# Optimization experiments

Measured on AMD Instinct MI355X. Metric: run time of the kernel, lower is better.

Reference implementation:

```python
import jax, jax.numpy as jnp
import numpy as np

BN_EPS = 1e-5


def knn_idx(x, k):
    # x: (B, N, C) -> (B, N, k) indices of k nearest neighbors (incl. self),
    # DGCNN style: topk of negative squared distance.
    inner = jnp.einsum('bnc,bmc->bnm', x, x)
    sq = jnp.sum(x * x, axis=-1)
    neg_dist = 2.0 * inner - sq[:, :, None] - sq[:, None, :]
    _, idx = jax.lax.top_k(neg_dist, k)
    return idx


def edge_conv(x, W, b, gamma, beta, k):
    # x: (B, N, C); W: (O, 2C). One DGCNN EdgeConv block:
    # knn gather -> concat(nbr - x, x) -> conv1x1 -> BN(batch stats) -> GELU -> max over k.
    idx = knn_idx(x, k)                                   # (B, N, k)
    nbr = jax.vmap(lambda f, i: f[i])(x, idx)             # (B, N, k, C)
    ctr = jnp.broadcast_to(x[:, :, None, :], nbr.shape)
    feat = jnp.concatenate([nbr - ctr, ctr], axis=-1)     # (B, N, k, 2C)
    y = jnp.einsum('bnkc,oc->bnko', feat, W) + b          # conv 1x1
    mean = jnp.mean(y, axis=(0, 1, 2))
    var = jnp.var(y, axis=(0, 1, 2))
    y = (y - mean) * jax.lax.rsqrt(var + BN_EPS) * gamma + beta
    y = jax.nn.gelu(y, approximate=False)                 # torch nn.GELU default (erf)
    return jnp.max(y, axis=2)                             # (B, N, O)


def setup_inputs() -> dict:
    key = jax.random.key(0)
    ks = jax.random.split(key, 8)
    bs, ch, n_patches, n_samples = 4, 6, 32, 256
    dims_in = [12, 32, 64, 128, 256]
    dims_out = [16, 32, 64, 128, 256]
    inp = {'x': jax.random.normal(ks[0], (bs, ch, n_patches, n_samples), dtype=jnp.float32)}
    for i, (ci, co) in enumerate(zip(dims_in, dims_out), start=1):
        wk = jax.random.fold_in(ks[1], i)
        scale = 1.0 / np.sqrt(ci)
        inp[f'W{i}'] = (jax.random.normal(wk, (co, ci), dtype=jnp.float32) * scale)
        inp[f'b{i}'] = jnp.zeros((co,), dtype=jnp.float32)
        inp[f'g{i}'] = jnp.ones((co,), dtype=jnp.float32)
        inp[f'bt{i}'] = jnp.zeros((co,), dtype=jnp.float32)
    inp['k'] = 16
    return inp


def reference(x, W1, b1, g1, bt1, W2, b2, g2, bt2, W3, b3, g3, bt3,
              W4, b4, g4, bt4, W5, b5, g5, bt5, k):
    bs, ch, n_patches, n_samples = x.shape
    # (bs, ch, P, S) -> (bs*P, S, ch)  [channels-last point clouds]
    h = x.transpose(0, 2, 3, 1).reshape(bs * n_patches, n_samples, ch)
    h = edge_conv(h, W1, b1, g1, bt1, k)
    h = edge_conv(h, W2, b2, g2, bt2, k)
    h = edge_conv(h, W3, b3, g3, bt3, k)
    h = edge_conv(h, W4, b4, g4, bt4, k)
    h = edge_conv(h, W5, b5, g5, bt5, k)      # (bs*P, S, dim)
    dim = h.shape[-1]
    h = h.reshape(bs, n_patches, n_samples, dim)
    return h.transpose(0, 3, 1, 2)            # (bs, dim, n_patches, n_samples)
```

## Files before the change

### kernel.cpp

```cpp
#include <hip/hip_runtime.h>
#include <cmath>

#define NPTS 256
#define TOTPTS 32768
#define KNB 16

static const size_t OFF_HA   = 0;
static const size_t OFF_HB   = 4194304;
static const size_t OFF_UZ   = 6291456;
static const size_t OFF_YMAX = 23068672;
static const size_t OFF_YMIN = 31457280;
static const size_t OFF_IDX  = 39845888;
static const size_t OFF_VT   = 40370176;
static const size_t OFF_SUMS = 40458240;

__device__ __forceinline__ float gelu_erf(float v) {
  return 0.5f * v * (1.0f + erff(v * 0.70710678118654752f));
}

__global__ __launch_bounds__(256) void prep_kernel(
    const float* __restrict__ x, float* __restrict__ h0,
    const float* __restrict__ W1, const float* __restrict__ W2, const float* __restrict__ W3,
    const float* __restrict__ W4, const float* __restrict__ W5,
    float* __restrict__ Vt, double* __restrict__ sums) {
  const int stride = gridDim.x * blockDim.x;
  const int tid0 = blockIdx.x * blockDim.x + threadIdx.x;
  for (int id = tid0; id < 196608; id += stride) {
    int ch = id % 6;
    int r  = id / 6;
    int s  = r & 255;
    int p  = (r >> 8) & 31;
    int bs = r >> 13;
    h0[id] = x[(((size_t)(bs * 6 + ch) * 32 + p) << 8) + s];
  }
  for (int id = tid0; id < 87232; id += stride) {
    const float* W; int K, N2, base;
    if (id < 192)        { W = W1; K = 6;   N2 = 32;  base = 0; }
    else if (id < 1216)  { W = W2; K = 16;  N2 = 64;  base = 192; }
    else if (id < 5312)  { W = W3; K = 32;  N2 = 128; base = 1216; }
    else if (id < 21696) { W = W4; K = 64;  N2 = 256; base = 5312; }
    else                 { W = W5; K = 128; N2 = 512; base = 21696; }
    int e = id - base;
    int c = e / N2;
    int j = e - c * N2;
    int O = N2 >> 1;
    Vt[id] = (j < O) ? W[j * 2 * K + c] : W[(j - O) * 2 * K + K + c];
  }
  for (int id = tid0; id < 992; id += stride) sums[id] = 0.0;
}

template<int C>
__global__ __launch_bounds__(256) void sq_kernel(const float* __restrict__ h,
                                                 double* __restrict__ sqd) {
  const int n = blockIdx.x * 256 + threadIdx.x;
  const float* p = h + (size_t)n * C;
  double q0 = 0.0, q1 = 0.0;
  #pragma unroll
  for (int c = 0; c + 1 < C; c += 2) {
    q0 = fma((double)p[c],   (double)p[c],   q0);
    q1 = fma((double)p[c+1], (double)p[c+1], q1);
  }
  #pragma unroll
  for (int c = C & ~1; c < C; ++c) q0 = fma((double)p[c], (double)p[c], q0);
  sqd[n] = q0 + q1;
}

template<int K>
__global__ __launch_bounds__(256) void knn_fused_kernel(const float* __restrict__ h,
                                                        const double* __restrict__ sqd,
                                                        int* __restrict__ idxout) {
  constexpr int KC  = (K < 16) ? K : 16;
  constexpr int AST = 18;
  constexpr int BST = 260;
  __shared__ __align__(16) float As[KC * AST];
  __shared__ __align__(16) float Bs[KC * BST];
  const int xcd   = blockIdx.x & 7;
  const int q     = blockIdx.x >> 3;
  const int cloud = xcd + 8 * (q >> 4);
  const int strip = q & 15;
  const int i0    = strip * 16;
  const float* hb = h + (size_t)cloud * NPTS * K;
  const int tid = threadIdx.x;
  const int c   = tid & 31;
  const int g   = tid >> 5;

  double acc[2][8];
  #pragma unroll
  for (int r = 0; r < 2; ++r)
    #pragma unroll
    for (int j = 0; j < 8; ++j) acc[r][j] = 0.0;

  for (int k0 = 0; k0 < K; k0 += KC) {
    if (K >= 16) {
      {
        int am = tid >> 4, ac = tid & 15;
        As[ac * AST + am] = hb[(size_t)(i0 + am) * K + k0 + ac];
      }
      #pragma unroll
      for (int qq = 0; qq < 4; ++qq) {
        int idx = tid + 256 * qq;
        int j  = idx >> 2;
        int kq = idx & 3;
        float4 v = *(const float4*)(hb + (size_t)j * K + k0 + 4 * kq);
        Bs[(4 * kq + 0) * BST + j] = v.x;
        Bs[(4 * kq + 1) * BST + j] = v.y;
        Bs[(4 * kq + 2) * BST + j] = v.z;
        Bs[(4 * kq + 3) * BST + j] = v.w;
      }
    } else {
      for (int e = tid; e < 16 * KC; e += 256) {
        int am = e / KC, ac = e - am * KC;
        As[ac * AST + am] = hb[(size_t)(i0 + am) * K + ac];
      }
      for (int e = tid; e < 256 * KC; e += 256) {
        int bm = e / KC, bc = e - bm * KC;
        Bs[bc * BST + bm] = hb[(size_t)bm * K + bc];
      }
    }
    __syncthreads();
    #pragma unroll
    for (int kk = 0; kk < KC; ++kk) {
      float2 af  = *(const float2*)(As + kk * AST + 2 * g);
      float4 bf0 = *(const float4*)(Bs + kk * BST + 4 * c);
      float4 bf1 = *(const float4*)(Bs + kk * BST + 128 + 4 * c);
      double a0 = (double)af.x, a1 = (double)af.y;
      double b0 = (double)bf0.x, b1 = (double)bf0.y, b2 = (double)bf0.z, b3 = (double)bf0.w;
      double b4 = (double)bf1.x, b5 = (double)bf1.y, b6 = (double)bf1.z, b7 = (double)bf1.w;
      acc[0][0] = fma(a0, b0, acc[0][0]);
      acc[0][1] = fma(a0, b1, acc[0][1]);
      acc[0][2] = fma(a0, b2, acc[0][2]);
      acc[0][3] = fma(a0, b3, acc[0][3]);
      acc[0][4] = fma(a0, b4, acc[0][4]);
      acc[0][5] = fma(a0, b5, acc[0][5]);
      acc[0][6] = fma(a0, b6, acc[0][6]);
      acc[0][7] = fma(a0, b7, acc[0][7]);
      acc[1][0] = fma(a1, b0, acc[1][0]);
      acc[1][1] = fma(a1, b1, acc[1][1]);
      acc[1][2] = fma(a1, b2, acc[1][2]);
      acc[1][3] = fma(a1, b3, acc[1][3]);
      acc[1][4] = fma(a1, b4, acc[1][4]);
      acc[1][5] = fma(a1, b5, acc[1][5]);
      acc[1][6] = fma(a1, b6, acc[1][6]);
      acc[1][7] = fma(a1, b7, acc[1][7]);
    }
    __syncthreads();
  }

  const double sqi0 = sqd[cloud * NPTS + i0 + 2 * g];
  const double sqi1 = sqd[cloud * NPTS + i0 + 2 * g + 1];
  double sqj[8];
  #pragma unroll
  for (int e = 0; e < 4; ++e) {
    sqj[e]     = sqd[cloud * NPTS + 4 * c + e];
    sqj[4 + e] = sqd[cloud * NPTS + 128 + 4 * c + e];
  }
  const unsigned cb0 = 4u * (unsigned)c;
  const unsigned cb1 = 128u + 4u * (unsigned)c;

  #define MK(P, COLV) ((((unsigned long long)__double_as_longlong(P)) & ~0xFFull) | (COLV))
  unsigned long long a0 = MK(2.0 * acc[0][0] - sqi0 - sqj[0], cb0 + 0u);
  unsigned long long a1 = MK(2.0 * acc[0][1] - sqi0 - sqj[1], cb0 + 1u);
  unsigned long long a2 = MK(2.0 * acc[0][2] - sqi0 - sqj[2], cb0 + 2u);
  unsigned long long a3 = MK(2.0 * acc[0][3] - sqi0 - sqj[3], cb0 + 3u);
  unsigned long long a4 = MK(2.0 * acc[0][4] - sqi0 - sqj[4], cb1 + 0u);
  unsigned long long a5 = MK(2.0 * acc[0][5] - sqi0 - sqj[5], cb1 + 1u);
  unsigned long long a6 = MK(2.0 * acc[0][6] - sqi0 - sqj[6], cb1 + 2u);
  unsigned long long a7 = MK(2.0 * acc[0][7] - sqi0 - sqj[7], cb1 + 3u);
  unsigned long long b0 = MK(2.0 * acc[1][0] - sqi1 - sqj[0], cb0 + 0u);
  unsigned long long b1 = MK(2.0 * acc[1][1] - sqi1 - sqj[1], cb0 + 1u);
  unsigned long long b2 = MK(2.0 * acc[1][2] - sqi1 - sqj[2], cb0 + 2u);
  unsigned long long b3 = MK(2.0 * acc[1][3] - sqi1 - sqj[3], cb0 + 3u);
  unsigned long long b4 = MK(2.0 * acc[1][4] - sqi1 - sqj[4], cb1 + 0u);
  unsigned long long b5 = MK(2.0 * acc[1][5] - sqi1 - sqj[5], cb1 + 1u);
  unsigned long long b6 = MK(2.0 * acc[1][6] - sqi1 - sqj[6], cb1 + 2u);
  unsigned long long b7 = MK(2.0 * acc[1][7] - sqi1 - sqj[7], cb1 + 3u);
  #undef MK

  #define CE(X, Y) { unsigned long long lo_ = (X < Y) ? X : Y; \
                     unsigned long long hi_ = (X < Y) ? Y : X; X = lo_; Y = hi_; }
  #define SORT8(v0,v1,v2,v3,v4,v5,v6,v7) \
    CE(v0,v1) CE(v2,v3) CE(v4,v5) CE(v6,v7) \
    CE(v0,v2) CE(v1,v3) CE(v4,v6) CE(v5,v7) \
    CE(v1,v2) CE(v5,v6) \
    CE(v0,v4) CE(v1,v5) CE(v2,v6) CE(v3,v7) \
    CE(v2,v4) CE(v3,v5) \
    CE(v1,v2) CE(v3,v4) CE(v5,v6)
  SORT8(a0,a1,a2,a3,a4,a5,a6,a7)
  SORT8(b0,b1,b2,b3,b4,b5,b6,b7)
  #undef SORT8
  #undef CE

  const unsigned long long FULL = 0xFFFFFFFFFFFFFFFFull;
  const int sub = c;
  int keep1 = 0, keep2 = 0;
  for (int round = 0; round < KNB; ++round) {
    unsigned long long m1 = a0, m2 = b0, o;
    o = __shfl_xor(m1, 16); m1 = (o < m1) ? o : m1;
    o = __shfl_xor(m2, 16); m2 = (o < m2) ? o : m2;
    o = __shfl_xor(m1, 8);  m1 = (o < m1) ? o : m1;
    o = __shfl_xor(m2, 8);  m2 = (o < m2) ? o : m2;
    o = __shfl_xor(m1, 4);  m1 = (o < m1) ? o : m1;
    o = __shfl_xor(m2, 4);  m2 = (o < m2) ? o : m2;
    o = __shfl_xor(m1, 2);  m1 = (o < m1) ? o : m1;
    o = __shfl_xor(m2, 2);  m2 = (o < m2) ? o : m2;
    o = __shfl_xor(m1, 1);  m1 = (o < m1) ? o : m1;
    o = __shfl_xor(m2, 1);  m2 = (o < m2) ? o : m2;
    const int col1 = (int)(m1 & 0xFFull);
    const int col2 = (int)(m2 & 0xFFull);
    if (((col1 >> 2) & 31) == sub) {
      a0 = a1; a1 = a2; a2 = a3; a3 = a4; a4 = a5; a5 = a6; a6 = a7; a7 = FULL;
    }
    if (((col2 >> 2) & 31) == sub) {
      b0 = b1; b1 = b2; b2 = b3; b3 = b4; b4 = b5; b5 = b6; b6 = b7; b7 = FULL;
    }
    if (sub == round) { keep1 = col1; keep2 = col2; }
  }
  if (sub < KNB) {
    const int rowA = cloud * NPTS + i0 + 2 * g;
    idxout[(size_t)rowA * KNB + sub]       = cloud * NPTS + keep1;
    idxout[(size_t)(rowA + 1) * KNB + sub] = cloud * NPTS + keep2;
  }
}

template<int K, int N2>
__global__ __launch_bounds__(256) void gemm_uz_kernel(const float* __restrict__ h,
                                                      const float* __restrict__ Vt,
                                                      float* __restrict__ UZ) {
  constexpr int KC = 32;
  constexpr int NBLK = (N2 + 63) / 64;
  __shared__ __align__(16) float As[KC * 68];
  __shared__ __align__(16) float Bs[KC * 68];
  const int m0 = (int)(blockIdx.x / NBLK) * 64;
  const int n0 = (int)(blockIdx.x % NBLK) * 64;
  const int tid = threadIdx.x;
  const int mm = (tid & 15) * 4;
  const int jj = (tid >> 4) * 4;
  float acc[4][4] = {{0.f}};
  for (int k0 = 0; k0 < K; k0 += KC) {
    #pragma unroll
    for (int e = tid; e < 64 * KC; e += 256) {
      int am = e / KC, ac = e - am * KC;
      float v = 0.f;
      if (k0 + ac < K) v = h[(size_t)(m0 + am) * K + k0 + ac];
      As[ac * 68 + am] = v;
    }
    #pragma unroll
    for (int e = tid; e < KC * 64; e += 256) {
      int bj = e & 63, bc = e >> 6;
      float v = 0.f;
      if (k0 + bc < K && n0 + bj < N2) v = Vt[(size_t)(k0 + bc) * N2 + n0 + bj];
      Bs[bc * 68 + bj] = v;
    }
    __syncthreads();
    #pragma unroll
    for (int c = 0; c < KC; ++c) {
      float4 av = *(const float4*)(As + c * 68 + mm);
      float4 bv = *(const float4*)(Bs + c * 68 + jj);
      acc[0][0] = fmaf(av.x, bv.x, acc[0][0]);
      acc[0][1] = fmaf(av.x, bv.y, acc[0][1]);
      acc[0][2] = fmaf(av.x, bv.z, acc[0][2]);
      acc[0][3] = fmaf(av.x, bv.w, acc[0][3]);
      acc[1][0] = fmaf(av.y, bv.x, acc[1][0]);
      acc[1][1] = fmaf(av.y, bv.y, acc[1][1]);
      acc[1][2] = fmaf(av.y, bv.z, acc[1][2]);
      acc[1][3] = fmaf(av.y, bv.w, acc[1][3]);
      acc[2][0] = fmaf(av.z, bv.x, acc[2][0]);
      acc[2][1] = fmaf(av.z, bv.y, acc[2][1]);
      acc[2][2] = fmaf(av.z, bv.z, acc[2][2]);
      acc[2][3] = fmaf(av.z, bv.w, acc[2][3]);
      acc[3][0] = fmaf(av.w, bv.x, acc[3][0]);
      acc[3][1] = fmaf(av.w, bv.y, acc[3][1]);
      acc[3][2] = fmaf(av.w, bv.z, acc[3][2]);
      acc[3][3] = fmaf(av.w, bv.w, acc[3][3]);
    }
    __syncthreads();
  }
  if (n0 + jj < N2) {
    #pragma unroll
    for (int i = 0; i < 4; ++i) {
      float4 v = make_float4(acc[i][0], acc[i][1], acc[i][2], acc[i][3]);
      *(float4*)(UZ + (size_t)(m0 + mm + i) * N2 + n0 + jj) = v;
    }
  }
}

template<int K, int N2>
__global__ __launch_bounds__(256) void gemm_big_kernel(const float* __restrict__ h,
                                                       const float* __restrict__ Vt,
                                                       float* __restrict__ UZ) {
  constexpr int KC = 32;
  constexpr int PAD = 132;
  constexpr int NBLK = N2 / 128;
  __shared__ __align__(16) float As[KC * PAD];
  __shared__ __align__(16) float Bs[KC * PAD];
  const int m0 = (int)(blockIdx.x / NBLK) * 128;
  const int n0 = (int)(blockIdx.x % NBLK) * 128;
  const int tid = threadIdx.x;
  const int ra = (tid & 15) * 4;
  const int ca = (tid >> 4) * 4;
  float acc[8][8];
  #pragma unroll
  for (int i = 0; i < 8; ++i)
    #pragma unroll
    for (int j = 0; j < 8; ++j) acc[i][j] = 0.f;

  for (int k0 = 0; k0 < K; k0 += KC) {
    #pragma unroll
    for (int q = 0; q < 4; ++q) {
      int idx = tid + 256 * q;
      int am = idx >> 3;
      int aq = idx & 7;
      float4 v = *(const float4*)(h + (size_t)(m0 + am) * K + k0 + 4 * aq);
      As[(4 * aq + 0) * PAD + am] = v.x;
      As[(4 * aq + 1) * PAD + am] = v.y;
      As[(4 * aq + 2) * PAD + am] = v.z;
      As[(4 * aq + 3) * PAD + am] = v.w;
    }
    #pragma unroll
    for (int q = 0; q < 4; ++q) {
      int idx = tid + 256 * q;
      int bk = idx >> 5;
      int bq = idx & 31;
      *(float4*)(Bs + bk * PAD + 4 * bq) =
          *(const float4*)(Vt + (size_t)(k0 + bk) * N2 + n0 + 4 * bq);
    }
    __syncthreads();
    #pragma unroll
    for (int cc = 0; cc < KC; ++cc) {
      float4 a0 = *(const float4*)(As + cc * PAD + ra);
      float4 a1 = *(const float4*)(As + cc * PAD + 64 + ra);
      float4 b0 = *(const float4*)(Bs + cc * PAD + ca);
      float4 b1 = *(const float4*)(Bs + cc * PAD + 64 + ca);
      float av[8] = {a0.x, a0.y, a0.z, a0.w, a1.x, a1.y, a1.z, a1.w};
      float bv[8] = {b0.x, b0.y, b0.z, b0.w, b1.x, b1.y, b1.z, b1.w};
      #pragma unroll
      for (int i = 0; i < 8; ++i)
        #pragma unroll
        for (int j = 0; j < 8; ++j)
          acc[i][j] = fmaf(av[i], bv[j], acc[i][j]);
    }
    __syncthreads();
  }
  #pragma unroll
  for (int i = 0; i < 8; ++i) {
    int row = m0 + ((i < 4) ? (ra + i) : (64 + ra + (i - 4)));
    float4 v0 = make_float4(acc[i][0], acc[i][1], acc[i][2], acc[i][3]);
    float4 v1 = make_float4(acc[i][4], acc[i][5], acc[i][6], acc[i][7]);
    *(float4*)(UZ + (size_t)row * N2 + n0 + ca) = v0;
    *(float4*)(UZ + (size_t)row * N2 + n0 + 64 + ca) = v1;
  }
}

template<int O, int GRID>
__global__ __launch_bounds__(256) void combine_kernel(const float* __restrict__ UZ,
    const int* __restrict__ idx, const float* __restrict__ bias,
    float* __restrict__ ymax, float* __restrict__ ymin, double* __restrict__ partials) {
  constexpr int TPP = O / 4;
  constexpr int PPI = 256 / TPP;
  constexpr int PPB = TOTPTS / GRID;
  constexpr int ITERS = PPB / PPI;
  static_assert(ITERS >= 1, "grid too large for this O");
  constexpr int BPC = GRID / 128;
  __shared__ double red[256];
  const int tid = threadIdx.x;
  const int oc  = tid % TPP;
  const int sub = tid / TPP;
  const int x    = blockIdx.x & 7;
  const int slot = blockIdx.x >> 3;
  const int c    = x + 8 * (slot / BPC);
  const int w    = slot % BPC;
  const int base = c * NPTS + w * PPB;
  const float4* UZ4 = (const float4*)UZ;
  float4* ymx4 = (float4*)ymax;
  float4* ymn4 = (float4*)ymin;
  const float4 b4 = ((const float4*)bias)[oc];
  double a1x = 0.0, a1y = 0.0, a1z = 0.0, a1w = 0.0;
  double a2x = 0.0, a2y = 0.0, a2z = 0.0, a2w = 0.0;
  for (int it = 0; it < ITERS; ++it) {
    int n = base + it * PPI + sub;
    const int* ip = idx + (size_t)n * KNB;
    float4 un = UZ4[(size_t)n * (O / 2) + oc];
    float4 zn = UZ4[(size_t)n * (O / 2) + O / 4 + oc];
    float4 w4 = make_float4(zn.x - un.x + b4.x, zn.y - un.y + b4.y,
                            zn.z - un.z + b4.z, zn.w - un.w + b4.w);
    float4 mx = make_float4(-INFINITY, -INFINITY, -INFINITY, -INFINITY);
    float4 mn = make_float4(INFINITY, INFINITY, INFINITY, INFINITY);
    float4 s1 = make_float4(0.f, 0.f, 0.f, 0.f);
    float4 s2 = make_float4(0.f, 0.f, 0.f, 0.f);
    #pragma unroll
    for (int kk = 0; kk < KNB; ++kk) {
      int j = ip[kk];
      float4 uv = UZ4[(size_t)j * (O / 2) + oc];
      mx.x = fmaxf(mx.x, uv.x); mx.y = fmaxf(mx.y, uv.y);
      mx.z = fmaxf(mx.z, uv.z); mx.w = fmaxf(mx.w, uv.w);
      mn.x = fminf(mn.x, uv.x); mn.y = fminf(mn.y, uv.y);
      mn.z = fminf(mn.z, uv.z); mn.w = fminf(mn.w, uv.w);
      s1.x += uv.x; s1.y += uv.y; s1.z += uv.z; s1.w += uv.w;
      s2.x = fmaf(uv.x, uv.x, s2.x); s2.y = fmaf(uv.y, uv.y, s2.y);
      s2.z = fmaf(uv.z, uv.z, s2.z); s2.w = fmaf(uv.w, uv.w, s2.w);
    }
    ymx4[(size_t)n * (O / 4) + oc] = make_float4(mx.x + w4.x, mx.y + w4.y, mx.z + w4.z, mx.w + w4.w);
    ymn4[(size_t)n * (O / 4) + oc] = make_float4(mn.x + w4.x, mn.y + w4.y, mn.z + w4.z, mn.w + w4.w);
    a1x += (double)(s1.x + 16.f * w4.x);
    a1y += (double)(s1.y + 16.f * w4.y);
    a1z += (double)(s1.z + 16.f * w4.z);
    a1w += (double)(s1.w + 16.f * w4.w);
    a2x += (double)(s2.x + 2.f * w4.x * s1.x + 16.f * (w4.x * w4.x));
    a2y += (double)(s2.y + 2.f * w4.y * s1.y + 16.f * (w4.y * w4.y));
    a2z += (double)(s2.z + 2.f * w4.z * s1.z + 16.f * (w4.z * w4.z));
    a2w += (double)(s2.w + 2.f * w4.w * s1.w + 16.f * (w4.w * w4.w));
  }
  #define REDUCE_ONE(VAL, CH_OFF)                                        \
    red[tid] = (VAL);                                                    \
    __syncthreads();                                                     \
    if (tid < TPP) {                                                     \
      double t = 0.0;                                                    \
      _Pragma("unroll")                                                  \
      for (int q = 0; q < PPI; ++q) t += red[q * TPP + tid];             \
      partials[(size_t)((CH_OFF) + 4 * tid) * GRID + blockIdx.x] = t;    \
    }                                                                    \
    __syncthreads();
  REDUCE_ONE(a1x, 0)
  REDUCE_ONE(a1y, 1)
  REDUCE_ONE(a1z, 2)
  REDUCE_ONE(a1w, 3)
  REDUCE_ONE(a2x, O + 0)
  REDUCE_ONE(a2y, O + 1)
  REDUCE_ONE(a2z, O + 2)
  REDUCE_ONE(a2w, O + 3)
  #undef REDUCE_ONE
}

template<int NB>
__global__ __launch_bounds__(256) void reduce_sums_kernel(const double* __restrict__ part,
                                                          double* __restrict__ sums) {
  __shared__ double red[256];
  const int ch = blockIdx.x;
  const double* p = part + (size_t)ch * NB;
  double t = 0.0;
  for (int i = threadIdx.x; i < NB; i += 256) t += p[i];
  red[threadIdx.x] = t;
  __syncthreads();
  #pragma unroll
  for (int s = 128; s > 0; s >>= 1) {
    if (threadIdx.x < s) red[threadIdx.x] += red[threadIdx.x + s];
    __syncthreads();
  }
  if (threadIdx.x == 0) sums[ch] = red[0];
}

template<int O>
__global__ __launch_bounds__(256) void apply_kernel(const float* __restrict__ ymax,
    const float* __restrict__ ymin, const double* __restrict__ sums,
    const float* __restrict__ g, const float* __restrict__ bt, float* __restrict__ hout) {
  const int tid = blockIdx.x * 256 + threadIdx.x;
  const int o = tid & (O - 1);
  double m = sums[o] * (1.0 / 524288.0);
  double v = fma(-m, m, sums[O + o] * (1.0 / 524288.0));
  float A = g[o] / sqrtf((float)v + 1e-5f);
  float Cc = fmaf(-(float)m, A, bt[o]);
  float r1 = gelu_erf(fmaf(A, ymax[tid], Cc));
  float r2 = gelu_erf(fmaf(A, ymin[tid], Cc));
  hout[tid] = fmaxf(r1, r2);
}

__global__ __launch_bounds__(256) void apply_final_kernel(const float* __restrict__ ymax,
    const float* __restrict__ ymin, const double* __restrict__ sums,
    const float* __restrict__ g, const float* __restrict__ bt, float* __restrict__ out) {
  constexpr int O = 256;
  __shared__ float tile[64 * 65];
  const int bo = blockIdx.x & 3;
  const int bn = blockIdx.x >> 2;
  const int n0 = bn * 64, o0 = bo * 64;
  const int lane = threadIdx.x & 63;
  const int grp = threadIdx.x >> 6;
  {
    const int oc = o0 + lane;
    double m = sums[oc] * (1.0 / 524288.0);
    double v = fma(-m, m, sums[O + oc] * (1.0 / 524288.0));
    float A = g[oc] / sqrtf((float)v + 1e-5f);
    float Cc = fmaf(-(float)m, A, bt[oc]);
    #pragma unroll
    for (int q = 0; q < 16; ++q) {
      int r = grp * 16 + q;
      size_t src = (size_t)(n0 + r) * O + oc;
      float r1 = gelu_erf(fmaf(A, ymax[src], Cc));
      float r2 = gelu_erf(fmaf(A, ymin[src], Cc));
      tile[r * 65 + lane] = fmaxf(r1, r2);
    }
  }
  __syncthreads();
  const int s0 = n0 & 255;
  const int p  = (n0 >> 8) & 31;
  const int bs = n0 >> 13;
  size_t basei = ((size_t)(bs * 256 + o0) * 32 + p) * 256 + s0;
  #pragma unroll
  for (int q = 0; q < 16; ++q) {
    int c = grp * 16 + q;
    out[basei + (size_t)c * 8192 + lane] = tile[lane * 65 + c];
  }
}

extern "C" void kernel_launch(void* const* d_in, const int* in_sizes, int n_in,
                              void* d_out, int out_size, void* d_ws, size_t ws_size,
                              hipStream_t stream) {
  (void)in_sizes; (void)n_in; (void)out_size; (void)ws_size;
  const float* x   = (const float*)d_in[0];
  const float* W1  = (const float*)d_in[1];
  const float* b1  = (const float*)d_in[2];
  const float* g1  = (const float*)d_in[3];
  const float* bt1 = (const float*)d_in[4];
  const float* W2  = (const float*)d_in[5];
  const float* b2  = (const float*)d_in[6];
  const float* g2  = (const float*)d_in[7];
  const float* bt2 = (const float*)d_in[8];
  const float* W3  = (const float*)d_in[9];
  const float* b3  = (const float*)d_in[10];
  const float* g3  = (const float*)d_in[11];
  const float* bt3 = (const float*)d_in[12];
  const float* W4  = (const float*)d_in[13];
  const float* b4  = (const float*)d_in[14];
  const float* g4  = (const float*)d_in[15];
  const float* bt4 = (const float*)d_in[16];
  const float* W5  = (const float*)d_in[17];
  const float* b5  = (const float*)d_in[18];
  const float* g5  = (const float*)d_in[19];
  const float* bt5 = (const float*)d_in[20];

  float* ws    = (float*)d_ws;
  float* hA    = ws + OFF_HA;
  float* hB    = ws + OFF_HB;
  float* UZ    = ws + OFF_UZ;
  float* ymx   = ws + OFF_YMAX;
  float* ymn   = ws + OFF_YMIN;
  int*   idxb  = (int*)(ws + OFF_IDX);
  float* Vt    = ws + OFF_VT;
  double* sums = (double*)(ws + OFF_SUMS);
  double* sqd  = (double*)ymx;
  double* partA = (double*)hA;
  double* partB = (double*)hB;

  static hipStream_t s2 = nullptr;
  static hipEvent_t evF[5], evJ[5];
  if (s2 == nullptr) {
    hipStreamCreateWithFlags(&s2, hipStreamNonBlocking);
    for (int i = 0; i < 5; ++i) {
      hipEventCreateWithFlags(&evF[i], hipEventDisableTiming);
      hipEventCreateWithFlags(&evJ[i], hipEventDisableTiming);
    }
  }

  #define FORK(l)  hipEventRecord(evF[l], stream); hipStreamWaitEvent(s2, evF[l], 0);
  #define JOIN(l)  hipEventRecord(evJ[l], s2);     hipStreamWaitEvent(stream, evJ[l], 0);

  prep_kernel<<<256, 256, 0, stream>>>(x, hA, W1, W2, W3, W4, W5, Vt, sums);

  FORK(0)
  gemm_uz_kernel<6, 32><<<512, 256, 0, s2>>>(hA, Vt + 0, UZ);
  sq_kernel<6><<<128, 256, 0, stream>>>(hA, sqd);
  knn_fused_kernel<6><<<2048, 256, 0, stream>>>(hA, sqd, idxb);
  JOIN(0)
  combine_kernel<16, 512><<<512, 256, 0, stream>>>(UZ, idxb, b1, ymx, ymn, partA);
  reduce_sums_kernel<512><<<32, 256, 0, stream>>>(partA, sums + 0);
  apply_kernel<16><<<2048, 256, 0, stream>>>(ymx, ymn, sums + 0, g1, bt1, hB);

  FORK(1)
  gemm_uz_kernel<16, 64><<<512, 256, 0, s2>>>(hB, Vt + 192, UZ);
  sq_kernel<16><<<128, 256, 0, stream>>>(hB, sqd);
  knn_fused_kernel<16><<<2048, 256, 0, stream>>>(hB, sqd, idxb);
  JOIN(1)
  combine_kernel<32, 1024><<<1024, 256, 0, stream>>>(UZ, idxb, b2, ymx, ymn, partB);
  reduce_sums_kernel<1024><<<64, 256, 0, stream>>>(partB, sums + 32);
  apply_kernel<32><<<4096, 256, 0, stream>>>(ymx, ymn, sums + 32, g2, bt2, hA);

  FORK(2)
  gemm_big_kernel<32, 128><<<256, 256, 0, s2>>>(hA, Vt + 1216, UZ);
  sq_kernel<32><<<128, 256, 0, stream>>>(hA, sqd);
  knn_fused_kernel<32><<<2048, 256, 0, stream>>>(hA, sqd, idxb);
  JOIN(2)
  combine_kernel<64, 2048><<<2048, 256, 0, stream>>>(UZ, idxb, b3, ymx, ymn, partA);
  reduce_sums_kernel<2048><<<128, 256, 0, stream>>>(partA, sums + 96);
  apply_kernel<64><<<8192, 256, 0, stream>>>(ymx, ymn, sums + 96, g3, bt3, hB);

  FORK(3)
  gemm_big_kernel<64, 256><<<512, 256, 0, s2>>>(hB, Vt + 5312, UZ);
  sq_kernel<64><<<128, 256, 0, stream>>>(hB, sqd);
  knn_fused_kernel<64><<<2048, 256, 0, stream>>>(hB, sqd, idxb);
  JOIN(3)
  combine_kernel<128, 2048><<<2048, 256, 0, stream>>>(UZ, idxb, b4, ymx, ymn, partB);
  reduce_sums_kernel<2048><<<256, 256, 0, stream>>>(partB, sums + 224);
  apply_kernel<128><<<16384, 256, 0, stream>>>(ymx, ymn, sums + 224, g4, bt4, hA);

  FORK(4)
  gemm_big_kernel<128, 512><<<1024, 256, 0, s2>>>(hA, Vt + 21696, UZ);
  sq_kernel<128><<<128, 256, 0, stream>>>(hA, sqd);
  knn_fused_kernel<128><<<2048, 256, 0, stream>>>(hA, sqd, idxb);
  JOIN(4)
  combine_kernel<256, 2048><<<2048, 256, 0, stream>>>(UZ, idxb, b5, ymx, ymn, partA);
  reduce_sums_kernel<2048><<<512, 256, 0, stream>>>(partA, sums + 480);
  apply_final_kernel<<<2048, 256, 0, stream>>>(ymx, ymn, sums + 480, g5, bt5, (float*)d_out);

  #undef FORK
  #undef JOIN
}
```

Baseline: 691.8 us.

## Extract two neighbors per top-k round and serialize GEMM before kNN

The warp-level top-k selection now merges the two smallest candidates per lane through a shuffle butterfly, popping up to two entries per round. This halves the number of selection rounds from 16 to 8 but does more compares and shuffles in each round. Separately, the JOIN for each layer moves to directly after the GEMM launch, so the GEMM on the side stream no longer overlaps sq/kNN and must finish before they start. That second change gives up concurrency, perhaps to avoid contention between the two streams.

Result: slower. 848.6 us (+22.7%).

```diff
diff --git a/kernel.cpp b/kernel.cpp
--- a/kernel.cpp
+++ b/kernel.cpp
@@ -193,27 +193,40 @@
   const unsigned long long FULL = 0xFFFFFFFFFFFFFFFFull;
   const int sub = c;
   int keep1 = 0, keep2 = 0;
-  for (int round = 0; round < KNB; ++round) {
-    unsigned long long m1 = a0, m2 = b0, o;
-    o = __shfl_xor(m1, 16); m1 = (o < m1) ? o : m1;
-    o = __shfl_xor(m2, 16); m2 = (o < m2) ? o : m2;
-    o = __shfl_xor(m1, 8);  m1 = (o < m1) ? o : m1;
-    o = __shfl_xor(m2, 8);  m2 = (o < m2) ? o : m2;
-    o = __shfl_xor(m1, 4);  m1 = (o < m1) ? o : m1;
-    o = __shfl_xor(m2, 4);  m2 = (o < m2) ? o : m2;
-    o = __shfl_xor(m1, 2);  m1 = (o < m1) ? o : m1;
-    o = __shfl_xor(m2, 2);  m2 = (o < m2) ? o : m2;
-    o = __shfl_xor(m1, 1);  m1 = (o < m1) ? o : m1;
-    o = __shfl_xor(m2, 1);  m2 = (o < m2) ? o : m2;
-    const int col1 = (int)(m1 & 0xFFull);
-    const int col2 = (int)(m2 & 0xFFull);
-    if (((col1 >> 2) & 31) == sub) {
+  for (int round = 0; round < 8; ++round) {
+    unsigned long long p0 = a0, p1 = a1;
+    unsigned long long r0 = b0, r1 = b1;
+    #define STEP2(M)                                                    \
+    {                                                                   \
+      unsigned long long q0_ = __shfl_xor(p0, M), q1_ = __shfl_xor(p1, M); \
+      unsigned long long s0_ = __shfl_xor(r0, M), s1_ = __shfl_xor(r1, M); \
+      unsigned long long hi1 = (p0 < q0_) ? q0_ : p0;                   \
+      p0 = (p0 < q0_) ? p0 : q0_;                                       \
+      unsigned long long mn1 = (p1 < q1_) ? p1 : q1_;                   \
+      p1 = (hi1 < mn1) ? hi1 : mn1;                                     \
+      unsigned long long hi2 = (r0 < s0_) ? s0_ : r0;                   \
+      r0 = (r0 < s0_) ? r0 : s0_;                                       \
+      unsigned long long mn2 = (r1 < s1_) ? r1 : s1_;                   \
+      r1 = (hi2 < mn2) ? hi2 : mn2;                                     \
+    }
+    STEP2(16) STEP2(8) STEP2(4) STEP2(2) STEP2(1)
+    #undef STEP2
+    const int c10 = (int)(p0 & 0xFFull), c11 = (int)(p1 & 0xFFull);
+    const int c20 = (int)(r0 & 0xFFull), c21 = (int)(r1 & 0xFFull);
+    const int pops1 = (((c10 >> 2) & 31) == sub ? 1 : 0) + (((c11 >> 2) & 31) == sub ? 1 : 0);
+    const int pops2 = (((c20 >> 2) & 31) == sub ? 1 : 0) + (((c21 >> 2) & 31) == sub ? 1 : 0);
+    if (pops1 == 2) {
+      a0 = a2; a1 = a3; a2 = a4; a3 = a5; a4 = a6; a5 = a7; a6 = FULL; a7 = FULL;
+    } else if (pops1 == 1) {
       a0 = a1; a1 = a2; a2 = a3; a3 = a4; a4 = a5; a5 = a6; a6 = a7; a7 = FULL;
     }
-    if (((col2 >> 2) & 31) == sub) {
+    if (pops2 == 2) {
+      b0 = b2; b1 = b3; b2 = b4; b3 = b5; b4 = b6; b5 = b7; b6 = FULL; b7 = FULL;
+    } else if (pops2 == 1) {
       b0 = b1; b1 = b2; b2 = b3; b3 = b4; b4 = b5; b5 = b6; b6 = b7; b7 = FULL;
     }
-    if (sub == round) { keep1 = col1; keep2 = col2; }
+    if (sub == 2 * round)     { keep1 = c10; keep2 = c20; }
+    if (sub == 2 * round + 1) { keep1 = c11; keep2 = c21; }
   }
   if (sub < KNB) {
     const int rowA = cloud * NPTS + i0 + 2 * g;
@@ -557,45 +570,45 @@
 
   FORK(0)
   gemm_uz_kernel<6, 32><<<512, 256, 0, s2>>>(hA, Vt + 0, UZ);
+  JOIN(0)
   sq_kernel<6><<<128, 256, 0, stream>>>(hA, sqd);
   knn_fused_kernel<6><<<2048, 256, 0, stream>>>(hA, sqd, idxb);
-  JOIN(0)
   combine_kernel<16, 512><<<512, 256, 0, stream>>>(UZ, idxb, b1, ymx, ymn, partA);
   reduce_sums_kernel<512><<<32, 256, 0, stream>>>(partA, sums + 0);
   apply_kernel<16><<<2048, 256, 0, stream>>>(ymx, ymn, sums + 0, g1, bt1, hB);
 
   FORK(1)
   gemm_uz_kernel<16, 64><<<512, 256, 0, s2>>>(hB, Vt + 192, UZ);
+  JOIN(1)
   sq_kernel<16><<<128, 256, 0, stream>>>(hB, sqd);
   knn_fused_kernel<16><<<2048, 256, 0, stream>>>(hB, sqd, idxb);
-  JOIN(1)
   combine_kernel<32, 1024><<<1024, 256, 0, stream>>>(UZ, idxb, b2, ymx, ymn, partB);
   reduce_sums_kernel<1024><<<64, 256, 0, stream>>>(partB, sums + 32);
   apply_kernel<32><<<4096, 256, 0, stream>>>(ymx, ymn, sums + 32, g2, bt2, hA);
 
   FORK(2)
   gemm_big_kernel<32, 128><<<256, 256, 0, s2>>>(hA, Vt + 1216, UZ);
+  JOIN(2)
   sq_kernel<32><<<128, 256, 0, stream>>>(hA, sqd);
   knn_fused_kernel<32><<<2048, 256, 0, stream>>>(hA, sqd, idxb);
-  JOIN(2)
   combine_kernel<64, 2048><<<2048, 256, 0, stream>>>(UZ, idxb, b3, ymx, ymn, partA);
   reduce_sums_kernel<2048><<<128, 256, 0, stream>>>(partA, sums + 96);
   apply_kernel<64><<<8192, 256, 0, stream>>>(ymx, ymn, sums + 96, g3, bt3, hB);
 
   FORK(3)
   gemm_big_kernel<64, 256><<<512, 256, 0, s2>>>(hB, Vt + 5312, UZ);
+  JOIN(3)
   sq_kernel<64><<<128, 256, 0, stream>>>(hB, sqd);
   knn_fused_kernel<64><<<2048, 256, 0, stream>>>(hB, sqd, idxb);
-  JOIN(3)
   combine_kernel<128, 2048><<<2048, 256, 0, stream>>>(UZ, idxb, b4, ymx, ymn, partB);
   reduce_sums_kernel<2048><<<256, 256, 0, stream>>>(partB, sums + 224);
   apply_kernel<128><<<16384, 256, 0, stream>>>(ymx, ymn, sums + 224, g4, bt4, hA);
 
   FORK(4)
   gemm_big_kernel<128, 512><<<1024, 256, 0, s2>>>(hA, Vt + 21696, UZ);
+  JOIN(4)
   sq_kernel<128><<<128, 256, 0, stream>>>(hA, sqd);
   knn_fused_kernel<128><<<2048, 256, 0, stream>>>(hA, sqd, idxb);
-  JOIN(4)
   combine_kernel<256, 2048><<<2048, 256, 0, stream>>>(UZ, idxb, b5, ymx, ymn, partA);
   reduce_sums_kernel<2048><<<512, 256, 0, stream>>>(partA, sums + 480);
   apply_final_kernel<<<2048, 256, 0, stream>>>(ymx, ymn, sums + 480, g5, bt5, (float*)d_out);
```
